# Optimization experiments

Measured on AMD Instinct MI355X. Metric: run time of the kernel, lower is better.

The kernel has to match this reference:

```python
import jax, jax.numpy as jnp
import numpy as np

N = 100000   # num nodes
E = 800000   # num edges
D = 16       # latent_dim
K = 3        # message-passing iterations
ALPHA = 0.1
GAMMA = 0.9


def _mlp2(x, w1, b1, w2, b2):
    return jax.nn.relu(x @ w1 + b1) @ w2 + b2


def setup_inputs() -> dict:
    key = jax.random.key(0)
    ks = iter(jax.random.split(key, 40))
    def w(shape, fan_in):
        return jax.random.normal(next(ks), shape, jnp.float32) / np.sqrt(fan_in)
    return {
        "edge_index": jax.random.randint(next(ks), (2, E), 0, N),
        "edge_attr": jax.random.normal(next(ks), (E, 3), jnp.float32),
        "a_ij": jax.random.normal(next(ks), (E, 1), jnp.float32),
        "prb_data": jax.random.normal(next(ks), (N, 1), jnp.float32),
        "sol": jax.random.normal(next(ks), (N, 1), jnp.float32),
        "y": jax.random.normal(next(ks), (N, 1), jnp.float32),
        "phi_to_w1": w((K, 2 * D + 3, D), 2 * D + 3), "phi_to_b1": jnp.zeros((K, D), jnp.float32),
        "phi_to_w2": w((K, D, D), D), "phi_to_b2": jnp.zeros((K, D), jnp.float32),
        "phi_from_w1": w((K, 2 * D + 3, D), 2 * D + 3), "phi_from_b1": jnp.zeros((K, D), jnp.float32),
        "phi_from_w2": w((K, D, D), D), "phi_from_b2": jnp.zeros((K, D), jnp.float32),
        "psi_w1": w((K, 3 * D + 1, D), 3 * D + 1), "psi_b1": jnp.zeros((K, D), jnp.float32),
        "psi_w2": w((K, D, D), D), "psi_b2": jnp.zeros((K, D), jnp.float32),
        "dec_w1": w((K, D, D), D), "dec_b1": jnp.zeros((K, D), jnp.float32),
        "dec_w2": w((K, D, 1), D), "dec_b2": jnp.zeros((K, 1), jnp.float32),
    }


def reference(edge_index, edge_attr, a_ij, prb_data, sol, y,
              phi_to_w1, phi_to_b1, phi_to_w2, phi_to_b2,
              phi_from_w1, phi_from_b1, phi_from_w2, phi_from_b2,
              psi_w1, psi_b1, psi_w2, psi_b2,
              dec_w1, dec_b1, dec_w2, dec_b2):
    src, dst = edge_index[0], edge_index[1]
    # remove_self_loops: with 'add' aggregation, zeroing self-loop messages is equivalent.
    sl_mask = (src != dst).astype(edge_attr.dtype)[:, None]

    def message_pass(h, xi_idx, xj_idx, agg_idx, w1, b1, w2, b2):
        # gather-concat-MLP-scatter: tmp is [E, 2D+3]
        tmp = jnp.concatenate([h[xi_idx], h[xj_idx], edge_attr], axis=1)
        m = _mlp2(tmp, w1, b1, w2, b2) * sl_mask
        return jax.ops.segment_sum(m, agg_idx, num_segments=N)

    a_val = a_ij[:, 0]
    def residual_loss(u):
        # SparseTensor(row=src, col=dst, value=a_ij) @ u  (self-loops kept here)
        Au = jax.ops.segment_sum(a_val * u[dst, 0], src, num_segments=N)[:, None]
        return jnp.mean((Au - y) ** 2)

    h = jnp.zeros((N, D), edge_attr.dtype)
    u = _mlp2(h, dec_w1[0], dec_b1[0], dec_w2[0], dec_b2[0])  # U['0']
    total_loss = jnp.zeros((), edge_attr.dtype)
    for t in range(K):
        # Phi_to: flow source_to_target -> x_i = h[dst], x_j = h[src], aggregate at dst
        mess_to = message_pass(h, dst, src, dst, phi_to_w1[t], phi_to_b1[t], phi_to_w2[t], phi_to_b2[t])
        # Phi_from: flow target_to_source -> x_i = h[src], x_j = h[dst], aggregate at src
        mess_from = message_pass(h, src, dst, src, phi_from_w1[t], phi_from_b1[t], phi_from_w2[t], phi_from_b2[t])
        concat = jnp.concatenate([h, mess_to, mess_from, prb_data], axis=1)  # [N, 3D+1]
        h = h + ALPHA * _mlp2(concat, psi_w1[t], psi_b1[t], psi_w2[t], psi_b2[t])
        u = _mlp2(h, dec_w1[t], dec_b1[t], dec_w2[t], dec_b2[t])
        total_loss = total_loss + residual_loss(u) * GAMMA ** (K - t - 1)
    return u, total_loss
```

## Files before the change

### kernel.cpp

```cpp
#include <hip/hip_runtime.h>

#define NN 100000
#define NE 800000
#define DD 16
#define ALPHA 0.1f

__device__ __forceinline__ void load16(const float* __restrict__ p, float* r) {
  float4 v0 = *(const float4*)(p + 0);
  float4 v1 = *(const float4*)(p + 4);
  float4 v2 = *(const float4*)(p + 8);
  float4 v3 = *(const float4*)(p + 12);
  r[0]=v0.x; r[1]=v0.y; r[2]=v0.z; r[3]=v0.w;
  r[4]=v1.x; r[5]=v1.y; r[6]=v1.z; r[7]=v1.w;
  r[8]=v2.x; r[9]=v2.y; r[10]=v2.z; r[11]=v2.w;
  r[12]=v3.x; r[13]=v3.y; r[14]=v3.z; r[15]=v3.w;
}

__device__ __forceinline__ void store16(float* __restrict__ p, const float* r) {
  *(float4*)(p + 0)  = make_float4(r[0], r[1], r[2], r[3]);
  *(float4*)(p + 4)  = make_float4(r[4], r[5], r[6], r[7]);
  *(float4*)(p + 8)  = make_float4(r[8], r[9], r[10], r[11]);
  *(float4*)(p + 12) = make_float4(r[12], r[13], r[14], r[15]);
}

__device__ __forceinline__ unsigned f2bf(float x) {
  unsigned b = __float_as_uint(x);
  return (b + 0x7FFFu + ((b >> 16) & 1u)) >> 16;
}

__global__ __launch_bounds__(256) void hist_kernel(
    const int* __restrict__ ei, int* __restrict__ hist,
    int* __restrict__ rank_dst, int* __restrict__ rank_src)
{
  int e = blockIdx.x * 256 + threadIdx.x;
  if (e >= NE) return;
  int s = ei[e];
  int d = ei[NE + e];
  rank_dst[e] = atomicAdd(&hist[d], 1);
  rank_src[e] = atomicAdd(&hist[NN + s], 1);
}

__global__ __launch_bounds__(256) void scan1_kernel(
    const int* __restrict__ in, int* __restrict__ out, int* __restrict__ sums, int L)
{
  __shared__ int sh[256];
  int t = threadIdx.x;
  int i0 = blockIdx.x * 1024 + t * 4;
  int v0 = (i0 + 0 < L) ? in[i0 + 0] : 0;
  int v1 = (i0 + 1 < L) ? in[i0 + 1] : 0;
  int v2 = (i0 + 2 < L) ? in[i0 + 2] : 0;
  int v3 = (i0 + 3 < L) ? in[i0 + 3] : 0;
  int tot = v0 + v1 + v2 + v3;
  sh[t] = tot;
  __syncthreads();
  int val = tot;
  for (int off = 1; off < 256; off <<= 1) {
    int x = (t >= off) ? sh[t - off] : 0;
    __syncthreads();
    val += x; sh[t] = val;
    __syncthreads();
  }
  if (t == 255) sums[blockIdx.x] = val;
  int run = val - tot;
  if (i0 + 0 < L) out[i0 + 0] = run; run += v0;
  if (i0 + 1 < L) out[i0 + 1] = run; run += v1;
  if (i0 + 2 < L) out[i0 + 2] = run; run += v2;
  if (i0 + 3 < L) out[i0 + 3] = run;
}

__global__ __launch_bounds__(256) void scan2_kernel(
    int* __restrict__ sums, int nb, int* __restrict__ out_total)
{
  __shared__ int sh[256];
  int t = threadIdx.x;
  int v = (t < nb) ? sums[t] : 0;
  sh[t] = v;
  __syncthreads();
  int val = v;
  for (int off = 1; off < 256; off <<= 1) {
    int x = (t >= off) ? sh[t - off] : 0;
    __syncthreads();
    val += x; sh[t] = val;
    __syncthreads();
  }
  if (t < nb) sums[t] = val - v;
  if (t == 255) *out_total = val;
}

__global__ __launch_bounds__(256) void scan3_kernel(
    int* __restrict__ out, const int* __restrict__ sums, int L)
{
  int i = blockIdx.x * 256 + threadIdx.x;
  if (i < L) out[i] += sums[i >> 10];
}

__global__ __launch_bounds__(256) void scatter_kernel(
    const int* __restrict__ ei, const float* __restrict__ ea, const float* __restrict__ a,
    const int* __restrict__ base,
    const int* __restrict__ rank_dst, const int* __restrict__ rank_src,
    float4* __restrict__ pay, float2* __restrict__ pay_au)
{
  int e = blockIdx.x * 256 + threadIdx.x;
  if (e >= NE) return;
  int s = ei[e];
  int d = ei[NE + e];
  float e0 = ea[3 * (size_t)e], e1 = ea[3 * (size_t)e + 1], e2 = ea[3 * (size_t)e + 2];
  int sl = (s == d);
  int pd = base[d] + rank_dst[e];
  pay[pd] = make_float4(__int_as_float(sl ? -1 : s), e0, e1, e2);
  int ps = base[NN + s] + rank_src[e];
  pay[ps] = make_float4(__int_as_float(sl ? -1 : d), e0, e1, e2);
  pay_au[ps - NE] = make_float2(__int_as_float(d), a[e]);
}

template<bool FIRST, bool WITH_AU>
__global__ __launch_bounds__(256) void gather_kernel(
    const float* __restrict__ h, const unsigned short* __restrict__ hb,
    const float4* __restrict__ pay, const int* __restrict__ base,
    const float* __restrict__ to_w1, const float* __restrict__ to_b1,
    const float* __restrict__ to_w2, const float* __restrict__ to_b2,
    const float* __restrict__ fr_w1, const float* __restrict__ fr_b1,
    const float* __restrict__ fr_w2, const float* __restrict__ fr_b2,
    float* __restrict__ mto, float* __restrict__ mfr, int gblocks,
    const float2* __restrict__ pay_au, const float* __restrict__ u,
    const float* __restrict__ y, float w, float* __restrict__ loss)
{
  if (WITH_AU && (int)blockIdx.x >= gblocks) {
    int n = (blockIdx.x - gblocks) * 256 + threadIdx.x;
    float acc = 0.0f;
    if (n < NN) {
      float au = 0.0f;
      int beg = base[NN + n] - NE, end = base[NN + n + 1] - NE;
      for (int i = beg; i < end; ++i) {
        float2 q = pay_au[i];
        au = fmaf(q.y, u[__float_as_int(q.x)], au);
      }
      float dlt = au - y[n];
      acc = dlt * dlt;
    }
    #pragma unroll
    for (int off = 32; off > 0; off >>= 1) acc += __shfl_down(acc, off);
    __shared__ float ss[4];
    int lane = threadIdx.x & 63, wid = threadIdx.x >> 6;
    if (lane == 0) ss[wid] = acc;
    __syncthreads();
    if (threadIdx.x == 0) atomicAdd(loss, (ss[0] + ss[1] + ss[2] + ss[3]) * w);
    return;
  }

  __shared__ float sw[1696];
  for (int i = threadIdx.x; i < 560; i += 256) { sw[i] = to_w1[i]; sw[848 + i] = fr_w1[i]; }
  { int i = threadIdx.x;
    if (i < 256) { sw[576 + i] = to_w2[i]; sw[848 + 576 + i] = fr_w2[i]; }
    if (i < 16) {
      sw[560 + i] = to_b1[i];
      sw[832 + i] = to_b2[i];
      sw[848 + 560 + i] = fr_b1[i];
      sw[848 + 832 + i] = fr_b2[i];
    }
  }
  __syncthreads();

  int gid = (blockIdx.x * 256 + threadIdx.x) >> 3;
  int l = threadIdx.x & 7;
  if (gid >= 2 * NN) return;
  int dir = (gid >= NN) ? 1 : 0;
  int n = gid - (dir ? NN : 0);

  const float* w1 = sw + (dir ? 848 : 0);
  const float* b1 = w1 + 560;
  const float* w2 = w1 + 576;
  const float* b2 = w1 + 832;

  float p1[DD];
  #pragma unroll
  for (int j = 0; j < DD; ++j) p1[j] = b1[j];
  if (!FIRST) {
    float hn[DD];
    load16(h + (size_t)n * DD, hn);
    #pragma unroll
    for (int i = 0; i < DD; ++i) {
      float x = hn[i];
      #pragma unroll
      for (int j = 0; j < DD; ++j) p1[j] = fmaf(x, w1[i * DD + j], p1[j]);
    }
  }

  float hs_[DD];
  #pragma unroll
  for (int j = 0; j < DD; ++j) hs_[j] = 0.0f;
  int cnt = 0;

  int beg = base[gid], end = base[gid + 1];
  for (int i = beg + l; i < end; i += 8) {
    float4 q = pay[i];
    int nb = __float_as_int(q.x);
    if (nb >= 0) {
      float hid[DD];
      #pragma unroll
      for (int j = 0; j < DD; ++j)
        hid[j] = fmaf(q.y, w1[32 * DD + j],
                 fmaf(q.z, w1[33 * DD + j],
                 fmaf(q.w, w1[34 * DD + j], p1[j])));
      if (!FIRST) {
        uint4 qa = *(const uint4*)(hb + (size_t)nb * DD);
        uint4 qb = *(const uint4*)(hb + (size_t)nb * DD + 8);
        float hv[DD];
        hv[0]  = __uint_as_float(qa.x << 16); hv[1]  = __uint_as_float(qa.x & 0xFFFF0000u);
        hv[2]  = __uint_as_float(qa.y << 16); hv[3]  = __uint_as_float(qa.y & 0xFFFF0000u);
        hv[4]  = __uint_as_float(qa.z << 16); hv[5]  = __uint_as_float(qa.z & 0xFFFF0000u);
        hv[6]  = __uint_as_float(qa.w << 16); hv[7]  = __uint_as_float(qa.w & 0xFFFF0000u);
        hv[8]  = __uint_as_float(qb.x << 16); hv[9]  = __uint_as_float(qb.x & 0xFFFF0000u);
        hv[10] = __uint_as_float(qb.y << 16); hv[11] = __uint_as_float(qb.y & 0xFFFF0000u);
        hv[12] = __uint_as_float(qb.z << 16); hv[13] = __uint_as_float(qb.z & 0xFFFF0000u);
        hv[14] = __uint_as_float(qb.w << 16); hv[15] = __uint_as_float(qb.w & 0xFFFF0000u);
        #pragma unroll
        for (int k = 0; k < DD; ++k) {
          float x = hv[k];
          #pragma unroll
          for (int j = 0; j < DD; ++j) hid[j] = fmaf(x, w1[(DD + k) * DD + j], hid[j]);
        }
      }
      #pragma unroll
      for (int j = 0; j < DD; ++j) hs_[j] += fmaxf(hid[j], 0.0f);
      ++cnt;
    }
  }

  #pragma unroll
  for (int j = 0; j < DD; ++j) {
    hs_[j] += __shfl_xor(hs_[j], 1, 64);
    hs_[j] += __shfl_xor(hs_[j], 2, 64);
    hs_[j] += __shfl_xor(hs_[j], 4, 64);
  }
  cnt += __shfl_xor(cnt, 1, 64);
  cnt += __shfl_xor(cnt, 2, 64);
  cnt += __shfl_xor(cnt, 4, 64);

  float c = (float)cnt;
  float m0 = c * b2[2 * l + 0];
  float m1 = c * b2[2 * l + 1];
  #pragma unroll
  for (int k = 0; k < DD; ++k) {
    float x = hs_[k];
    m0 = fmaf(x, w2[k * DD + 2 * l + 0], m0);
    m1 = fmaf(x, w2[k * DD + 2 * l + 1], m1);
  }
  float* dst = (dir ? mfr : mto) + (size_t)n * DD + 2 * l;
  *(float2*)dst = make_float2(m0, m1);
}

__global__ __launch_bounds__(256) void node_kernel(
    float* __restrict__ h, unsigned short* __restrict__ hb,
    const float* __restrict__ mto, const float* __restrict__ mfr,
    const float* __restrict__ prb,
    const float* __restrict__ psi_w1, const float* __restrict__ psi_b1,
    const float* __restrict__ psi_w2, const float* __restrict__ psi_b2,
    const float* __restrict__ dec_w1, const float* __restrict__ dec_b1,
    const float* __restrict__ dec_w2, const float* __restrict__ dec_b2,
    float* __restrict__ u)
{
  __shared__ float sw[1361];
  for (int i = threadIdx.x; i < 784; i += 256) sw[i] = psi_w1[i];
  { int i = threadIdx.x;
    if (i < 256) { sw[800 + i] = psi_w2[i]; sw[1072 + i] = dec_w1[i]; }
    if (i < 16) {
      sw[784 + i] = psi_b1[i];
      sw[1056 + i] = psi_b2[i];
      sw[1328 + i] = dec_b1[i];
      sw[1344 + i] = dec_w2[i];
    }
    if (i == 0) sw[1360] = dec_b2[0];
  }
  __syncthreads();

  int n = blockIdx.x * 256 + threadIdx.x;
  if (n >= NN) return;

  float hv[DD], mt[DD], mf[DD];
  load16(h + (size_t)n * DD, hv);
  load16(mto + (size_t)n * DD, mt);
  load16(mfr + (size_t)n * DD, mf);
  float p = prb[n];

  float hid[DD];
  #pragma unroll
  for (int j = 0; j < DD; ++j) hid[j] = sw[784 + j];
  #pragma unroll
  for (int i = 0; i < DD; ++i) {
    float x = hv[i];
    #pragma unroll
    for (int j = 0; j < DD; ++j) hid[j] = fmaf(x, sw[i * DD + j], hid[j]);
  }
  #pragma unroll
  for (int i = 0; i < DD; ++i) {
    float x = mt[i];
    #pragma unroll
    for (int j = 0; j < DD; ++j) hid[j] = fmaf(x, sw[(DD + i) * DD + j], hid[j]);
  }
  #pragma unroll
  for (int i = 0; i < DD; ++i) {
    float x = mf[i];
    #pragma unroll
    for (int j = 0; j < DD; ++j) hid[j] = fmaf(x, sw[(2 * DD + i) * DD + j], hid[j]);
  }
  #pragma unroll
  for (int j = 0; j < DD; ++j) hid[j] = fmaf(p, sw[48 * DD + j], hid[j]);
  #pragma unroll
  for (int j = 0; j < DD; ++j) hid[j] = fmaxf(hid[j], 0.0f);

  float hnew[DD];
  #pragma unroll
  for (int j = 0; j < DD; ++j) hnew[j] = sw[1056 + j];
  #pragma unroll
  for (int i = 0; i < DD; ++i) {
    float x = hid[i];
    #pragma unroll
    for (int j = 0; j < DD; ++j) hnew[j] = fmaf(x, sw[800 + i * DD + j], hnew[j]);
  }
  #pragma unroll
  for (int j = 0; j < DD; ++j) hnew[j] = fmaf(ALPHA, hnew[j], hv[j]);
  store16(h + (size_t)n * DD, hnew);

  uint4 pa, pb;
  pa.x = f2bf(hnew[0])  | (f2bf(hnew[1])  << 16);
  pa.y = f2bf(hnew[2])  | (f2bf(hnew[3])  << 16);
  pa.z = f2bf(hnew[4])  | (f2bf(hnew[5])  << 16);
  pa.w = f2bf(hnew[6])  | (f2bf(hnew[7])  << 16);
  pb.x = f2bf(hnew[8])  | (f2bf(hnew[9])  << 16);
  pb.y = f2bf(hnew[10]) | (f2bf(hnew[11]) << 16);
  pb.z = f2bf(hnew[12]) | (f2bf(hnew[13]) << 16);
  pb.w = f2bf(hnew[14]) | (f2bf(hnew[15]) << 16);
  *(uint4*)(hb + (size_t)n * DD)     = pa;
  *(uint4*)(hb + (size_t)n * DD + 8) = pb;

  float hid2[DD];
  #pragma unroll
  for (int j = 0; j < DD; ++j) hid2[j] = sw[1328 + j];
  #pragma unroll
  for (int i = 0; i < DD; ++i) {
    float x = hnew[i];
    #pragma unroll
    for (int j = 0; j < DD; ++j) hid2[j] = fmaf(x, sw[1072 + i * DD + j], hid2[j]);
  }
  float uo = sw[1360];
  #pragma unroll
  for (int i = 0; i < DD; ++i) uo += fmaxf(hid2[i], 0.0f) * sw[1344 + i];
  u[n] = uo;
}

extern "C" void kernel_launch(void* const* d_in, const int* in_sizes, int n_in,
                              void* d_out, int out_size, void* d_ws, size_t ws_size,
                              hipStream_t stream) {
  const int*   ei        = (const int*)d_in[0];
  const float* ea        = (const float*)d_in[1];
  const float* a_ij      = (const float*)d_in[2];
  const float* prb       = (const float*)d_in[3];
  const float* y         = (const float*)d_in[5];
  const float* phi_to_w1 = (const float*)d_in[6];
  const float* phi_to_b1 = (const float*)d_in[7];
  const float* phi_to_w2 = (const float*)d_in[8];
  const float* phi_to_b2 = (const float*)d_in[9];
  const float* phi_fr_w1 = (const float*)d_in[10];
  const float* phi_fr_b1 = (const float*)d_in[11];
  const float* phi_fr_w2 = (const float*)d_in[12];
  const float* phi_fr_b2 = (const float*)d_in[13];
  const float* psi_w1    = (const float*)d_in[14];
  const float* psi_b1    = (const float*)d_in[15];
  const float* psi_w2    = (const float*)d_in[16];
  const float* psi_b2    = (const float*)d_in[17];
  const float* dec_w1    = (const float*)d_in[18];
  const float* dec_b1    = (const float*)d_in[19];
  const float* dec_w2    = (const float*)d_in[20];
  const float* dec_b2    = (const float*)d_in[21];

  float* out_u    = (float*)d_out;
  float* out_loss = out_u + NN;

  char* wp = (char*)d_ws;
  auto carve = [&](size_t bytes) { void* p = (void*)wp; wp += (bytes + 15) & ~(size_t)15; return p; };
  float4* pay      = (float4*)carve((size_t)2 * NE * 16);
  float2* pay_au   = (float2*)carve((size_t)NE * 8);
  float*  h        = (float*)carve((size_t)NN * DD * 4);
  unsigned short* hb16 = (unsigned short*)carve((size_t)NN * DD * 2);
  float*  mto      = (float*)carve((size_t)NN * DD * 4);
  float*  mfr      = (float*)carve((size_t)NN * DD * 4);
  int*    rank_dst = (int*)carve((size_t)NE * 4);
  int*    rank_src = (int*)carve((size_t)NE * 4);
  int*    base     = (int*)carve((size_t)(2 * NN + 1) * 4);
  int*    hist     = (int*)carve((size_t)2 * NN * 4);
  int*    sums     = (int*)carve(256 * 4);

  hipMemsetAsync(h, 0, (size_t)NN * DD * 4, stream);
  hipMemsetAsync(out_loss, 0, 4, stream);
  hipMemsetAsync(hist, 0, (size_t)2 * NN * 4, stream);

  const int EB  = (NE + 255) / 256;
  const int NB  = (NN + 255) / 256;
  const int L2N = 2 * NN;
  const int SB1 = (L2N + 1023) / 1024;
  const int SB3 = (L2N + 255) / 256;
  const int GB8 = (L2N * 8 + 255) / 256;

  hist_kernel<<<EB, 256, 0, stream>>>(ei, hist, rank_dst, rank_src);
  scan1_kernel<<<SB1, 256, 0, stream>>>(hist, base, sums, L2N);
  scan2_kernel<<<1, 256, 0, stream>>>(sums, SB1, base + L2N);
  scan3_kernel<<<SB3, 256, 0, stream>>>(base, sums, L2N);
  scatter_kernel<<<EB, 256, 0, stream>>>(ei, ea, a_ij, base, rank_dst, rank_src,
                                         pay, pay_au);

  const float gw[3] = {0.81f, 0.9f, 1.0f};

  gather_kernel<true, false><<<GB8, 256, 0, stream>>>(
      h, hb16, pay, base,
      phi_to_w1, phi_to_b1, phi_to_w2, phi_to_b2,
      phi_fr_w1, phi_fr_b1, phi_fr_w2, phi_fr_b2,
      mto, mfr, GB8, pay_au, out_u, y, 0.0f, out_loss);
  node_kernel<<<NB, 256, 0, stream>>>(
      h, hb16, mto, mfr, prb,
      psi_w1, psi_b1, psi_w2, psi_b2,
      dec_w1, dec_b1, dec_w2, dec_b2, out_u);

  for (int t = 1; t < 3; ++t) {
    gather_kernel<false, true><<<GB8 + NB, 256, 0, stream>>>(
        h, hb16, pay, base,
        phi_to_w1 + t * 560, phi_to_b1 + t * 16, phi_to_w2 + t * 256, phi_to_b2 + t * 16,
        phi_fr_w1 + t * 560, phi_fr_b1 + t * 16, phi_fr_w2 + t * 256, phi_fr_b2 + t * 16,
        mto, mfr, GB8, pay_au, out_u, y, gw[t - 1] / (float)NN, out_loss);
    node_kernel<<<NB, 256, 0, stream>>>(
        h, hb16, mto, mfr, prb,
        psi_w1 + t * 784, psi_b1 + t * 16, psi_w2 + t * 256, psi_b2 + t * 16,
        dec_w1 + t * 256, dec_b1 + t * 16, dec_w2 + t * 16, dec_b2 + t, out_u);
  }

  gather_kernel<false, true><<<NB, 256, 0, stream>>>(
      h, hb16, pay, base,
      phi_to_w1, phi_to_b1, phi_to_w2, phi_to_b2,
      phi_fr_w1, phi_fr_b1, phi_fr_w2, phi_fr_b2,
      mto, mfr, 0, pay_au, out_u, y, gw[2] / (float)NN, out_loss);
}
```

Baseline: 341.8 us.

## Process gather edges block-wide with shared-memory atomic aggregation per node tile

Replaces the 8-lanes-per-node gather with a block that owns 256 consecutive nodes. Its threads stride over the block's contiguous CSR edge range and accumulate ReLU hidden sums into shared memory with atomics. This targets load imbalance across variable-degree nodes and underused lanes. The per-node first-layer projection is precomputed once into shared memory, and the edge payload packs the local node index and a self-loop flag into the neighbour word. Rank arrays shrink to 16 bits. The cost is heavy shared-memory atomic traffic and much larger LDS use per block, which lowers occupancy.

```diff
diff --git a/kernel.cpp b/kernel.cpp
--- a/kernel.cpp
+++ b/kernel.cpp
@@ -4,6 +4,7 @@
 #define NE 800000
 #define DD 16
 #define ALPHA 0.1f
+#define NB0 391
 
 __device__ __forceinline__ void load16(const float* __restrict__ p, float* r) {
   float4 v0 = *(const float4*)(p + 0);
@@ -30,14 +31,14 @@
 
 __global__ __launch_bounds__(256) void hist_kernel(
     const int* __restrict__ ei, int* __restrict__ hist,
-    int* __restrict__ rank_dst, int* __restrict__ rank_src)
+    unsigned short* __restrict__ rank_dst, unsigned short* __restrict__ rank_src)
 {
   int e = blockIdx.x * 256 + threadIdx.x;
   if (e >= NE) return;
   int s = ei[e];
   int d = ei[NE + e];
-  rank_dst[e] = atomicAdd(&hist[d], 1);
-  rank_src[e] = atomicAdd(&hist[NN + s], 1);
+  rank_dst[e] = (unsigned short)atomicAdd(&hist[d], 1);
+  rank_src[e] = (unsigned short)atomicAdd(&hist[NN + s], 1);
 }
 
 __global__ __launch_bounds__(256) void scan1_kernel(
@@ -97,26 +98,32 @@
 __global__ __launch_bounds__(256) void scatter_kernel(
     const int* __restrict__ ei, const float* __restrict__ ea, const float* __restrict__ a,
     const int* __restrict__ base,
-    const int* __restrict__ rank_dst, const int* __restrict__ rank_src,
-    float4* __restrict__ pay, float2* __restrict__ pay_au)
+    const unsigned short* __restrict__ rank_dst, const unsigned short* __restrict__ rank_src,
+    uint4* __restrict__ pay, float2* __restrict__ pay_au)
 {
   int e = blockIdx.x * 256 + threadIdx.x;
   if (e >= NE) return;
   int s = ei[e];
   int d = ei[NE + e];
-  float e0 = ea[3 * (size_t)e], e1 = ea[3 * (size_t)e + 1], e2 = ea[3 * (size_t)e + 2];
-  int sl = (s == d);
+  unsigned u0 = __float_as_uint(ea[3 * (size_t)e]);
+  unsigned u1 = __float_as_uint(ea[3 * (size_t)e + 1]);
+  unsigned u2 = __float_as_uint(ea[3 * (size_t)e + 2]);
+  unsigned slbit = (s == d) ? (1u << 17) : 0u;
+
   int pd = base[d] + rank_dst[e];
-  pay[pd] = make_float4(__int_as_float(sl ? -1 : s), e0, e1, e2);
+  unsigned pxd = (slbit ? slbit : (unsigned)s) | ((unsigned)(d & 255) << 18);
+  pay[pd] = make_uint4(pxd, u0, u1, u2);
+
   int ps = base[NN + s] + rank_src[e];
-  pay[ps] = make_float4(__int_as_float(sl ? -1 : d), e0, e1, e2);
+  unsigned pxs = (slbit ? slbit : (unsigned)d) | ((unsigned)(s & 255) << 18);
+  pay[ps] = make_uint4(pxs, u0, u1, u2);
   pay_au[ps - NE] = make_float2(__int_as_float(d), a[e]);
 }
 
 template<bool FIRST, bool WITH_AU>
 __global__ __launch_bounds__(256) void gather_kernel(
     const float* __restrict__ h, const unsigned short* __restrict__ hb,
-    const float4* __restrict__ pay, const int* __restrict__ base,
+    const uint4* __restrict__ pay, const int* __restrict__ base,
     const float* __restrict__ to_w1, const float* __restrict__ to_b1,
     const float* __restrict__ to_w2, const float* __restrict__ to_b2,
     const float* __restrict__ fr_w1, const float* __restrict__ fr_b1,
@@ -125,8 +132,15 @@
     const float2* __restrict__ pay_au, const float* __restrict__ u,
     const float* __restrict__ y, float w, float* __restrict__ loss)
 {
+  __shared__ float sw[848];
+  __shared__ float p1s[256 * 17];
+  __shared__ float accs[256 * 17];
+  __shared__ float ss[4];
+
+  int t = threadIdx.x;
+
   if (WITH_AU && (int)blockIdx.x >= gblocks) {
-    int n = (blockIdx.x - gblocks) * 256 + threadIdx.x;
+    int n = (blockIdx.x - gblocks) * 256 + t;
     float acc = 0.0f;
     if (n < NN) {
       float au = 0.0f;
@@ -140,114 +154,106 @@
     }
     #pragma unroll
     for (int off = 32; off > 0; off >>= 1) acc += __shfl_down(acc, off);
-    __shared__ float ss[4];
-    int lane = threadIdx.x & 63, wid = threadIdx.x >> 6;
+    int lane = t & 63, wid = t >> 6;
     if (lane == 0) ss[wid] = acc;
     __syncthreads();
-    if (threadIdx.x == 0) atomicAdd(loss, (ss[0] + ss[1] + ss[2] + ss[3]) * w);
+    if (t == 0) atomicAdd(loss, (ss[0] + ss[1] + ss[2] + ss[3]) * w);
     return;
   }
 
-  __shared__ float sw[1696];
-  for (int i = threadIdx.x; i < 560; i += 256) { sw[i] = to_w1[i]; sw[848 + i] = fr_w1[i]; }
-  { int i = threadIdx.x;
-    if (i < 256) { sw[576 + i] = to_w2[i]; sw[848 + 576 + i] = fr_w2[i]; }
-    if (i < 16) {
-      sw[560 + i] = to_b1[i];
-      sw[832 + i] = to_b2[i];
-      sw[848 + 560 + i] = fr_b1[i];
-      sw[848 + 832 + i] = fr_b2[i];
+  int b = blockIdx.x;
+  int dir = (b >= NB0) ? 1 : 0;
+  int n0 = (dir ? (b - NB0) : b) * 256;
+  int n1 = min(n0 + 256, NN);
+  int gid0 = dir * NN + n0;
+  int ebeg = base[gid0];
+  int eend = base[dir * NN + n1];
+
+  {
+    const float* w1p = dir ? fr_w1 : to_w1;
+    const float* w2p = dir ? fr_w2 : to_w2;
+    const float* b1p = dir ? fr_b1 : to_b1;
+    const float* b2p = dir ? fr_b2 : to_b2;
+    for (int i = t; i < 560; i += 256) sw[i] = w1p[i];
+    if (t < 256) sw[576 + t] = w2p[t];
+    if (t < 16) { sw[560 + t] = b1p[t]; sw[832 + t] = b2p[t]; }
+  }
+  for (int i = t; i < 256 * 17; i += 256) accs[i] = 0.0f;
+  __syncthreads();
+
+  if (t < n1 - n0) {
+    float pv[DD];
+    #pragma unroll
+    for (int j = 0; j < DD; ++j) pv[j] = sw[560 + j];
+    if (!FIRST) {
+      float hv[DD];
+      load16(h + (size_t)(n0 + t) * DD, hv);
+      #pragma unroll
+      for (int k = 0; k < DD; ++k) {
+        float x = hv[k];
+        #pragma unroll
+        for (int j = 0; j < DD; ++j) pv[j] = fmaf(x, sw[k * DD + j], pv[j]);
+      }
     }
-  }
-  __syncthreads();
-
-  int gid = (blockIdx.x * 256 + threadIdx.x) >> 3;
-  int l = threadIdx.x & 7;
-  if (gid >= 2 * NN) return;
-  int dir = (gid >= NN) ? 1 : 0;
-  int n = gid - (dir ? NN : 0);
-
-  const float* w1 = sw + (dir ? 848 : 0);
-  const float* b1 = w1 + 560;
-  const float* w2 = w1 + 576;
-  const float* b2 = w1 + 832;
-
-  float p1[DD];
-  #pragma unroll
-  for (int j = 0; j < DD; ++j) p1[j] = b1[j];
-  if (!FIRST) {
-    float hn[DD];
-    load16(h + (size_t)n * DD, hn);
-    #pragma unroll
-    for (int i = 0; i < DD; ++i) {
-      float x = hn[i];
+    #pragma unroll
+    for (int j = 0; j < DD; ++j) p1s[t * 17 + j] = pv[j];
+  }
+  __syncthreads();
+
+  for (int i = ebeg + t; i < eend; i += 256) {
+    uint4 q = pay[i];
+    unsigned px = q.x;
+    if (px & (1u << 17)) continue;
+    int gl = px >> 18;
+    float a0 = __uint_as_float(q.y), a1 = __uint_as_float(q.z), a2 = __uint_as_float(q.w);
+
+    float hid[DD];
+    #pragma unroll
+    for (int j = 0; j < DD; ++j)
+      hid[j] = fmaf(a0, sw[512 + j],
+               fmaf(a1, sw[528 + j],
+               fmaf(a2, sw[544 + j], p1s[gl * 17 + j])));
+
+    if (!FIRST) {
+      int nbr = px & 0x1FFFF;
+      uint4 qa = *(const uint4*)(hb + (size_t)nbr * DD);
+      uint4 qb = *(const uint4*)(hb + (size_t)nbr * DD + 8);
+      float hv[DD];
+      hv[0]  = __uint_as_float(qa.x << 16); hv[1]  = __uint_as_float(qa.x & 0xFFFF0000u);
+      hv[2]  = __uint_as_float(qa.y << 16); hv[3]  = __uint_as_float(qa.y & 0xFFFF0000u);
+      hv[4]  = __uint_as_float(qa.z << 16); hv[5]  = __uint_as_float(qa.z & 0xFFFF0000u);
+      hv[6]  = __uint_as_float(qa.w << 16); hv[7]  = __uint_as_float(qa.w & 0xFFFF0000u);
+      hv[8]  = __uint_as_float(qb.x << 16); hv[9]  = __uint_as_float(qb.x & 0xFFFF0000u);
+      hv[10] = __uint_as_float(qb.y << 16); hv[11] = __uint_as_float(qb.y & 0xFFFF0000u);
+      hv[12] = __uint_as_float(qb.z << 16); hv[13] = __uint_as_float(qb.z & 0xFFFF0000u);
+      hv[14] = __uint_as_float(qb.w << 16); hv[15] = __uint_as_float(qb.w & 0xFFFF0000u);
       #pragma unroll
-      for (int j = 0; j < DD; ++j) p1[j] = fmaf(x, w1[i * DD + j], p1[j]);
+      for (int k = 0; k < DD; ++k) {
+        float x = hv[k];
+        #pragma unroll
+        for (int j = 0; j < DD; ++j) hid[j] = fmaf(x, sw[(DD + k) * DD + j], hid[j]);
+      }
     }
-  }
-
-  float hs_[DD];
-  #pragma unroll
-  for (int j = 0; j < DD; ++j) hs_[j] = 0.0f;
-  int cnt = 0;
-
-  int beg = base[gid], end = base[gid + 1];
-  for (int i = beg + l; i < end; i += 8) {
-    float4 q = pay[i];
-    int nb = __float_as_int(q.x);
-    if (nb >= 0) {
-      float hid[DD];
+
+    #pragma unroll
+    for (int j = 0; j < DD; ++j) atomicAdd(&accs[gl * 17 + j], fmaxf(hid[j], 0.0f));
+    atomicAdd(&accs[gl * 17 + 16], 1.0f);
+  }
+  __syncthreads();
+
+  if (t < n1 - n0) {
+    float c = accs[t * 17 + 16];
+    float ms[DD];
+    #pragma unroll
+    for (int j = 0; j < DD; ++j) ms[j] = c * sw[832 + j];
+    #pragma unroll
+    for (int k = 0; k < DD; ++k) {
+      float x = accs[t * 17 + k];
       #pragma unroll
-      for (int j = 0; j < DD; ++j)
-        hid[j] = fmaf(q.y, w1[32 * DD + j],
-                 fmaf(q.z, w1[33 * DD + j],
-                 fmaf(q.w, w1[34 * DD + j], p1[j])));
-      if (!FIRST) {
-        uint4 qa = *(const uint4*)(hb + (size_t)nb * DD);
-        uint4 qb = *(const uint4*)(hb + (size_t)nb * DD + 8);
-        float hv[DD];
-        hv[0]  = __uint_as_float(qa.x << 16); hv[1]  = __uint_as_float(qa.x & 0xFFFF0000u);
-        hv[2]  = __uint_as_float(qa.y << 16); hv[3]  = __uint_as_float(qa.y & 0xFFFF0000u);
-        hv[4]  = __uint_as_float(qa.z << 16); hv[5]  = __uint_as_float(qa.z & 0xFFFF0000u);
-        hv[6]  = __uint_as_float(qa.w << 16); hv[7]  = __uint_as_float(qa.w & 0xFFFF0000u);
-        hv[8]  = __uint_as_float(qb.x << 16); hv[9]  = __uint_as_float(qb.x & 0xFFFF0000u);
-        hv[10] = __uint_as_float(qb.y << 16); hv[11] = __uint_as_float(qb.y & 0xFFFF0000u);
-        hv[12] = __uint_as_float(qb.z << 16); hv[13] = __uint_as_float(qb.z & 0xFFFF0000u);
-        hv[14] = __uint_as_float(qb.w << 16); hv[15] = __uint_as_float(qb.w & 0xFFFF0000u);
-        #pragma unroll
-        for (int k = 0; k < DD; ++k) {
-          float x = hv[k];
-          #pragma unroll
-          for (int j = 0; j < DD; ++j) hid[j] = fmaf(x, w1[(DD + k) * DD + j], hid[j]);
-        }
-      }
-      #pragma unroll
-      for (int j = 0; j < DD; ++j) hs_[j] += fmaxf(hid[j], 0.0f);
-      ++cnt;
+      for (int j = 0; j < DD; ++j) ms[j] = fmaf(x, sw[576 + k * DD + j], ms[j]);
     }
-  }
-
-  #pragma unroll
-  for (int j = 0; j < DD; ++j) {
-    hs_[j] += __shfl_xor(hs_[j], 1, 64);
-    hs_[j] += __shfl_xor(hs_[j], 2, 64);
-    hs_[j] += __shfl_xor(hs_[j], 4, 64);
-  }
-  cnt += __shfl_xor(cnt, 1, 64);
-  cnt += __shfl_xor(cnt, 2, 64);
-  cnt += __shfl_xor(cnt, 4, 64);
-
-  float c = (float)cnt;
-  float m0 = c * b2[2 * l + 0];
-  float m1 = c * b2[2 * l + 1];
-  #pragma unroll
-  for (int k = 0; k < DD; ++k) {
-    float x = hs_[k];
-    m0 = fmaf(x, w2[k * DD + 2 * l + 0], m0);
-    m1 = fmaf(x, w2[k * DD + 2 * l + 1], m1);
-  }
-  float* dst = (dir ? mfr : mto) + (size_t)n * DD + 2 * l;
-  *(float2*)dst = make_float2(m0, m1);
+    store16((dir ? mfr : mto) + (size_t)(n0 + t) * DD, ms);
+  }
 }
 
 __global__ __launch_bounds__(256) void node_kernel(
@@ -379,14 +385,14 @@
 
   char* wp = (char*)d_ws;
   auto carve = [&](size_t bytes) { void* p = (void*)wp; wp += (bytes + 15) & ~(size_t)15; return p; };
-  float4* pay      = (float4*)carve((size_t)2 * NE * 16);
+  uint4*  pay      = (uint4*)carve((size_t)2 * NE * 16);
   float2* pay_au   = (float2*)carve((size_t)NE * 8);
   float*  h        = (float*)carve((size_t)NN * DD * 4);
   unsigned short* hb16 = (unsigned short*)carve((size_t)NN * DD * 2);
   float*  mto      = (float*)carve((size_t)NN * DD * 4);
   float*  mfr      = (float*)carve((size_t)NN * DD * 4);
-  int*    rank_dst = (int*)carve((size_t)NE * 4);
-  int*    rank_src = (int*)carve((size_t)NE * 4);
+  unsigned short* rank_dst = (unsigned short*)carve((size_t)NE * 2);
+  unsigned short* rank_src = (unsigned short*)carve((size_t)NE * 2);
   int*    base     = (int*)carve((size_t)(2 * NN + 1) * 4);
   int*    hist     = (int*)carve((size_t)2 * NN * 4);
   int*    sums     = (int*)carve(256 * 4);
@@ -400,7 +406,7 @@
   const int L2N = 2 * NN;
   const int SB1 = (L2N + 1023) / 1024;
   const int SB3 = (L2N + 255) / 256;
-  const int GB8 = (L2N * 8 + 255) / 256;
+  const int GBK = 2 * NB0;
 
   hist_kernel<<<EB, 256, 0, stream>>>(ei, hist, rank_dst, rank_src);
   scan1_kernel<<<SB1, 256, 0, stream>>>(hist, base, sums, L2N);
@@ -411,22 +417,22 @@
 
   const float gw[3] = {0.81f, 0.9f, 1.0f};
 
-  gather_kernel<true, false><<<GB8, 256, 0, stream>>>(
+  gather_kernel<true, false><<<GBK, 256, 0, stream>>>(
       h, hb16, pay, base,
       phi_to_w1, phi_to_b1, phi_to_w2, phi_to_b2,
       phi_fr_w1, phi_fr_b1, phi_fr_w2, phi_fr_b2,
-      mto, mfr, GB8, pay_au, out_u, y, 0.0f, out_loss);
+      mto, mfr, GBK, pay_au, out_u, y, 0.0f, out_loss);
   node_kernel<<<NB, 256, 0, stream>>>(
       h, hb16, mto, mfr, prb,
       psi_w1, psi_b1, psi_w2, psi_b2,
       dec_w1, dec_b1, dec_w2, dec_b2, out_u);
 
   for (int t = 1; t < 3; ++t) {
-    gather_kernel<false, true><<<GB8 + NB, 256, 0, stream>>>(
+    gather_kernel<false, true><<<GBK + NB, 256, 0, stream>>>(
         h, hb16, pay, base,
         phi_to_w1 + t * 560, phi_to_b1 + t * 16, phi_to_w2 + t * 256, phi_to_b2 + t * 16,
         phi_fr_w1 + t * 560, phi_fr_b1 + t * 16, phi_fr_w2 + t * 256, phi_fr_b2 + t * 16,
-        mto, mfr, GB8, pay_au, out_u, y, gw[t - 1] / (float)NN, out_loss);
+        mto, mfr, GBK, pay_au, out_u, y, gw[t - 1] / (float)NN, out_loss);
     node_kernel<<<NB, 256, 0, stream>>>(
         h, hb16, mto, mfr, prb,
         psi_w1 + t * 784, psi_b1 + t * 16, psi_w2 + t * 256, psi_b2 + t * 16,
```

Measured after the change: 983.9 us. 2.88x slower.

## Sort gather groups by degree and split per-node projection across lanes

Applied to the files above, without the earlier changes.

Adds a counting sort of the 2N (node, direction) segments by degree, clamped at 63, through three new kernels. The gather kernel reads segments through this permutation, so the 8-lane groups in a wavefront handle similar edge counts and lose less time to divergence. It also spreads the h[n]·W1 projection over the 8 lanes, two outputs per lane, and shares the results through LDS, instead of each lane computing all 16 redundantly. The cost is three extra setup launches, scattered node access order that may hurt locality of h and base, and an extra __syncthreads in the gather kernel.

```diff
diff --git a/kernel.cpp b/kernel.cpp
--- a/kernel.cpp
+++ b/kernel.cpp
@@ -113,10 +113,62 @@
   pay_au[ps - NE] = make_float2(__int_as_float(d), a[e]);
 }
 
+__global__ __launch_bounds__(256) void dbucket_kernel(
+    const int* __restrict__ base, int* __restrict__ dhist)
+{
+  __shared__ int lh[64];
+  int t = threadIdx.x;
+  if (t < 64) lh[t] = 0;
+  __syncthreads();
+  int g = blockIdx.x * 256 + t;
+  if (g < 2 * NN) {
+    int dg = base[g + 1] - base[g];
+    atomicAdd(&lh[min(dg, 63)], 1);
+  }
+  __syncthreads();
+  if (t < 64 && lh[t]) atomicAdd(&dhist[t], lh[t]);
+}
+
+__global__ void dscan64_kernel(int* __restrict__ dhist)
+{
+  int t = threadIdx.x;
+  int v = dhist[t];
+  int x = v;
+  #pragma unroll
+  for (int off = 1; off < 64; off <<= 1) {
+    int y = __shfl_up(x, off, 64);
+    if (t >= off) x += y;
+  }
+  dhist[t] = x - v;
+}
+
+__global__ __launch_bounds__(256) void dperm_kernel(
+    const int* __restrict__ base, int* __restrict__ dhist, int* __restrict__ perm)
+{
+  __shared__ int lh[64];
+  __shared__ int lb[64];
+  int t = threadIdx.x;
+  if (t < 64) lh[t] = 0;
+  __syncthreads();
+  int g = blockIdx.x * 256 + t;
+  int b = 0, r = 0;
+  bool v = (g < 2 * NN);
+  if (v) {
+    int dg = base[g + 1] - base[g];
+    b = min(dg, 63);
+    r = atomicAdd(&lh[b], 1);
+  }
+  __syncthreads();
+  if (t < 64 && lh[t]) lb[t] = atomicAdd(&dhist[t], lh[t]);
+  __syncthreads();
+  if (v) perm[lb[b] + r] = g;
+}
+
 template<bool FIRST, bool WITH_AU>
 __global__ __launch_bounds__(256) void gather_kernel(
     const float* __restrict__ h, const unsigned short* __restrict__ hb,
     const float4* __restrict__ pay, const int* __restrict__ base,
+    const int* __restrict__ perm,
     const float* __restrict__ to_w1, const float* __restrict__ to_b1,
     const float* __restrict__ to_w2, const float* __restrict__ to_b2,
     const float* __restrict__ fr_w1, const float* __restrict__ fr_b1,
@@ -126,6 +178,7 @@
     const float* __restrict__ y, float w, float* __restrict__ loss)
 {
   if (WITH_AU && (int)blockIdx.x >= gblocks) {
+    __shared__ float ss[4];
     int n = (blockIdx.x - gblocks) * 256 + threadIdx.x;
     float acc = 0.0f;
     if (n < NN) {
@@ -140,7 +193,6 @@
     }
     #pragma unroll
     for (int off = 32; off > 0; off >>= 1) acc += __shfl_down(acc, off);
-    __shared__ float ss[4];
     int lane = threadIdx.x & 63, wid = threadIdx.x >> 6;
     if (lane == 0) ss[wid] = acc;
     __syncthreads();
@@ -149,8 +201,10 @@
   }
 
   __shared__ float sw[1696];
-  for (int i = threadIdx.x; i < 560; i += 256) { sw[i] = to_w1[i]; sw[848 + i] = fr_w1[i]; }
-  { int i = threadIdx.x;
+  __shared__ float p1buf[512];
+  int t = threadIdx.x;
+  for (int i = t; i < 560; i += 256) { sw[i] = to_w1[i]; sw[848 + i] = fr_w1[i]; }
+  { int i = t;
     if (i < 256) { sw[576 + i] = to_w2[i]; sw[848 + 576 + i] = fr_w2[i]; }
     if (i < 16) {
       sw[560 + i] = to_b1[i];
@@ -161,29 +215,37 @@
   }
   __syncthreads();
 
-  int gid = (blockIdx.x * 256 + threadIdx.x) >> 3;
-  int l = threadIdx.x & 7;
-  if (gid >= 2 * NN) return;
-  int dir = (gid >= NN) ? 1 : 0;
-  int n = gid - (dir ? NN : 0);
+  int sub = (blockIdx.x * 256 + t) >> 3;
+  int l = t & 7;
+  int g = perm[sub];
+  int dir = (g >= NN) ? 1 : 0;
+  int n = g - (dir ? NN : 0);
 
   const float* w1 = sw + (dir ? 848 : 0);
   const float* b1 = w1 + 560;
   const float* w2 = w1 + 576;
   const float* b2 = w1 + 832;
 
-  float p1[DD];
-  #pragma unroll
-  for (int j = 0; j < DD; ++j) p1[j] = b1[j];
-  if (!FIRST) {
-    float hn[DD];
-    load16(h + (size_t)n * DD, hn);
-    #pragma unroll
-    for (int i = 0; i < DD; ++i) {
-      float x = hn[i];
-      #pragma unroll
-      for (int j = 0; j < DD; ++j) p1[j] = fmaf(x, w1[i * DD + j], p1[j]);
+  float p1v[DD];
+  if (FIRST) {
+    #pragma unroll
+    for (int j = 0; j < DD; ++j) p1v[j] = b1[j];
+  } else {
+    float hv[DD];
+    load16(h + (size_t)n * DD, hv);
+    int j0 = 2 * l;
+    float pa = b1[j0], pb = b1[j0 + 1];
+    #pragma unroll
+    for (int k = 0; k < DD; ++k) {
+      pa = fmaf(hv[k], w1[k * DD + j0], pa);
+      pb = fmaf(hv[k], w1[k * DD + j0 + 1], pb);
     }
+    p1buf[2 * t] = pa;
+    p1buf[2 * t + 1] = pb;
+    __syncthreads();
+    const float* pbase = &p1buf[(t & ~7) * 2];
+    #pragma unroll
+    for (int j = 0; j < DD; ++j) p1v[j] = pbase[j];
   }
 
   float hs_[DD];
@@ -191,7 +253,7 @@
   for (int j = 0; j < DD; ++j) hs_[j] = 0.0f;
   int cnt = 0;
 
-  int beg = base[gid], end = base[gid + 1];
+  int beg = base[g], end = base[g + 1];
   for (int i = beg + l; i < end; i += 8) {
     float4 q = pay[i];
     int nb = __float_as_int(q.x);
@@ -201,7 +263,7 @@
       for (int j = 0; j < DD; ++j)
         hid[j] = fmaf(q.y, w1[32 * DD + j],
                  fmaf(q.z, w1[33 * DD + j],
-                 fmaf(q.w, w1[34 * DD + j], p1[j])));
+                 fmaf(q.w, w1[34 * DD + j], p1v[j])));
       if (!FIRST) {
         uint4 qa = *(const uint4*)(hb + (size_t)nb * DD);
         uint4 qb = *(const uint4*)(hb + (size_t)nb * DD + 8);
@@ -390,17 +452,21 @@
   int*    base     = (int*)carve((size_t)(2 * NN + 1) * 4);
   int*    hist     = (int*)carve((size_t)2 * NN * 4);
   int*    sums     = (int*)carve(256 * 4);
+  int*    dhist    = (int*)carve(64 * 4);
+  int*    perm     = rank_dst;
 
   hipMemsetAsync(h, 0, (size_t)NN * DD * 4, stream);
   hipMemsetAsync(out_loss, 0, 4, stream);
   hipMemsetAsync(hist, 0, (size_t)2 * NN * 4, stream);
+  hipMemsetAsync(dhist, 0, 64 * 4, stream);
 
   const int EB  = (NE + 255) / 256;
   const int NB  = (NN + 255) / 256;
   const int L2N = 2 * NN;
   const int SB1 = (L2N + 1023) / 1024;
   const int SB3 = (L2N + 255) / 256;
-  const int GB8 = (L2N * 8 + 255) / 256;
+  const int DB  = (L2N + 255) / 256;
+  const int GB8 = (L2N * 8) / 256;
 
   hist_kernel<<<EB, 256, 0, stream>>>(ei, hist, rank_dst, rank_src);
   scan1_kernel<<<SB1, 256, 0, stream>>>(hist, base, sums, L2N);
@@ -408,11 +474,14 @@
   scan3_kernel<<<SB3, 256, 0, stream>>>(base, sums, L2N);
   scatter_kernel<<<EB, 256, 0, stream>>>(ei, ea, a_ij, base, rank_dst, rank_src,
                                          pay, pay_au);
+  dbucket_kernel<<<DB, 256, 0, stream>>>(base, dhist);
+  dscan64_kernel<<<1, 64, 0, stream>>>(dhist);
+  dperm_kernel<<<DB, 256, 0, stream>>>(base, dhist, perm);
 
   const float gw[3] = {0.81f, 0.9f, 1.0f};
 
   gather_kernel<true, false><<<GB8, 256, 0, stream>>>(
-      h, hb16, pay, base,
+      h, hb16, pay, base, perm,
       phi_to_w1, phi_to_b1, phi_to_w2, phi_to_b2,
       phi_fr_w1, phi_fr_b1, phi_fr_w2, phi_fr_b2,
       mto, mfr, GB8, pay_au, out_u, y, 0.0f, out_loss);
@@ -423,7 +492,7 @@
 
   for (int t = 1; t < 3; ++t) {
     gather_kernel<false, true><<<GB8 + NB, 256, 0, stream>>>(
-        h, hb16, pay, base,
+        h, hb16, pay, base, perm,
         phi_to_w1 + t * 560, phi_to_b1 + t * 16, phi_to_w2 + t * 256, phi_to_b2 + t * 16,
         phi_fr_w1 + t * 560, phi_fr_b1 + t * 16, phi_fr_w2 + t * 256, phi_fr_b2 + t * 16,
         mto, mfr, GB8, pay_au, out_u, y, gw[t - 1] / (float)NN, out_loss);
@@ -434,7 +503,7 @@
   }
 
   gather_kernel<false, true><<<NB, 256, 0, stream>>>(
-      h, hb16, pay, base,
+      h, hb16, pay, base, perm,
       phi_to_w1, phi_to_b1, phi_to_w2, phi_to_b2,
       phi_fr_w1, phi_fr_b1, phi_fr_w2, phi_fr_b2,
       mto, mfr, 0, pay_au, out_u, y, gw[2] / (float)NN, out_loss);
```

After: 343.0 us. Within noise of the previous version (+0.3%).
